# Kernel tuning notes

Measured on AMD Instinct MI355X. Metric: run time of the kernel, lower is better.

Reference implementation:

```python
import jax, jax.numpy as jnp
import numpy as np

D_MODEL = 1024
NUM_HEADS = 16
D_K = D_MODEL // NUM_HEADS
B, S = 4, 2048
NEG = -1e9


def setup_inputs() -> dict:
    key = jax.random.key(0)
    ks = jax.random.split(key, 12)
    def lin(kw, kb):
        bound = 1.0 / np.sqrt(D_MODEL)
        W = jax.random.uniform(kw, (D_MODEL, D_MODEL), jnp.float32, -bound, bound)
        b = jax.random.uniform(kb, (D_MODEL,), jnp.float32, -bound, bound)
        return W, b
    Wq, bq = lin(ks[0], ks[1])
    Wk, bk = lin(ks[2], ks[3])
    Wv, bv = lin(ks[4], ks[5])
    Wo, bo = lin(ks[6], ks[7])
    Q = jax.random.normal(ks[8], (B, S, D_MODEL), jnp.float32)
    K = jax.random.normal(ks[9], (B, S, D_MODEL), jnp.float32)
    V = jax.random.normal(ks[10], (B, S, D_MODEL), jnp.float32)
    # causal mask: 1 = keep, 0 = masked
    mask = jnp.tril(jnp.ones((S, S), jnp.int32))[None, None, :, :]
    mask = jnp.broadcast_to(mask, (B, 1, S, S))
    return {"Q": Q, "K": K, "V": V, "mask": mask,
            "Wq": Wq, "bq": bq, "Wk": Wk, "bk": bk,
            "Wv": Wv, "bv": bv, "Wo": Wo, "bo": bo}


def _split_heads(x):
    b, s, _ = x.shape
    return x.reshape(b, s, NUM_HEADS, D_K).transpose(0, 2, 1, 3)  # [B,H,S,Dk]


def reference(Q, K, V, mask, Wq, bq, Wk, bk, Wv, bv, Wo, bo):
    q = _split_heads(Q @ Wq.T + bq)
    k = _split_heads(K @ Wk.T + bk)
    v = _split_heads(V @ Wv.T + bv)
    scores = jnp.einsum('bhqd,bhkd->bhqk', q, k) / jnp.sqrt(jnp.float32(D_K))
    scores = jnp.where(mask == 0, jnp.float32(NEG), scores)
    probs = jax.nn.softmax(scores, axis=-1)
    attn = jnp.einsum('bhqk,bhkd->bhqd', probs, v)  # [B,H,S,Dk]
    attn = attn.transpose(0, 2, 1, 3).reshape(Q.shape[0], Q.shape[1], D_MODEL)
    return attn @ Wo.T + bo
```

## Files before the change

kernel.cpp:

```cpp
#include <hip/hip_runtime.h>
#include <hip/hip_bf16.h>
#include <cstdint>

typedef float floatx4 __attribute__((ext_vector_type(4)));
typedef __bf16 bf16x8 __attribute__((ext_vector_type(8)));

#define AS_G __attribute__((address_space(1)))
#define AS_L __attribute__((address_space(3)))

__device__ __forceinline__ void async_cp16(const void* g, void* l) {
    __builtin_amdgcn_global_load_lds((const AS_G uint32_t*)g, (AS_L uint32_t*)l, 16, 0, 0);
}

__device__ __forceinline__ floatx4 mfma16x16x32(bf16x8 a, bf16x8 b, floatx4 c) {
    return __builtin_amdgcn_mfma_f32_16x16x32_bf16(a, b, c, 0, 0, 0);
}

__device__ __forceinline__ unsigned short f2bf(float x) {
    return __builtin_bit_cast(unsigned short, (__bf16)x);
}

__global__ __launch_bounds__(256) void cvt4_f32_bf16(const float* __restrict__ a, const float* __restrict__ b,
                                                     const float* __restrict__ c, const float* __restrict__ d,
                                                     unsigned short* __restrict__ out, int n) {
    const float* in = blockIdx.y == 0 ? a : blockIdx.y == 1 ? b : blockIdx.y == 2 ? c : d;
    unsigned short* o = out + (size_t)blockIdx.y * n;
    int i = (blockIdx.x * 256 + threadIdx.x) * 4;
    if (i >= n) return;
    float4 v = *(const float4*)(in + i);
    ushort4 u;
    u.x = f2bf(v.x); u.y = f2bf(v.y); u.z = f2bf(v.z); u.w = f2bf(v.w);
    *(ushort4*)(o + i) = u;
}

__global__ __launch_bounds__(256) void cvt3_f32_bf16(const float* __restrict__ q, const float* __restrict__ k,
                                                     const float* __restrict__ v,
                                                     unsigned short* __restrict__ oq, unsigned short* __restrict__ ok,
                                                     unsigned short* __restrict__ ov, int n) {
    const float* in = blockIdx.y == 0 ? q : blockIdx.y == 1 ? k : v;
    unsigned short* o = blockIdx.y == 0 ? oq : blockIdx.y == 1 ? ok : ov;
    int i = (blockIdx.x * 256 + threadIdx.x) * 4;
    if (i >= n) return;
    float4 f = *(const float4*)(in + i);
    ushort4 u;
    u.x = f2bf(f.x); u.y = f2bf(f.y); u.z = f2bf(f.z); u.w = f2bf(f.w);
    *(ushort4*)(o + i) = u;
}

__device__ __forceinline__ void gemm_core(const unsigned short* __restrict__ A,
                                          const unsigned short* __restrict__ W,
                                          unsigned short* __restrict__ As,
                                          unsigned short* __restrict__ Bs,
                                          int m0, int n0, int wave, int lane,
                                          floatx4 (&acc)[4][4]) {
    const int quad = lane >> 4, l15 = lane & 15;
    const int l7   = l15 & 7;
    const int waveM = (wave >> 1) * 64, waveN = (wave & 1) * 64;
    const int r8  = lane >> 3;
    const int gsw = (lane & 7) ^ r8;

    for (int k0 = 0; k0 < 1024; k0 += 64) {
        for (int c = wave; c < 16; c += 4) {
            const int row = c * 8 + r8;
            async_cp16(A + (size_t)(m0 + row) * 1024 + k0 + gsw * 8, (char*)As + c * 1024);
            async_cp16(W + (size_t)(n0 + row) * 1024 + k0 + gsw * 8, (char*)Bs + c * 1024);
        }
        __syncthreads();

#pragma unroll
        for (int h = 0; h < 2; ++h) {
            const int g = (quad + h * 4) ^ l7;
            bf16x8 af[4], bf[4];
#pragma unroll
            for (int t = 0; t < 4; ++t) {
                af[t] = *(const bf16x8*)&As[(waveM + t * 16 + l15) * 64 + g * 8];
                bf[t] = *(const bf16x8*)&Bs[(waveN + t * 16 + l15) * 64 + g * 8];
            }
#pragma unroll
            for (int mt = 0; mt < 4; ++mt)
#pragma unroll
                for (int nt = 0; nt < 4; ++nt)
                    acc[mt][nt] = mfma16x16x32(af[mt], bf[nt], acc[mt][nt]);
        }
        __syncthreads();
    }
}

__global__ __launch_bounds__(256) void gemm_qkv(const unsigned short* __restrict__ Aq,
                                                const unsigned short* __restrict__ Ak,
                                                const unsigned short* __restrict__ Av,
                                                const unsigned short* __restrict__ wb,
                                                const float* __restrict__ bqp, const float* __restrict__ bkp,
                                                const float* __restrict__ bvp,
                                                float qscl,
                                                unsigned short* __restrict__ qp, unsigned short* __restrict__ kp,
                                                unsigned short* __restrict__ vtp) {
    __shared__ unsigned short As[128 * 64];
    __shared__ unsigned short Bs[128 * 64];
    const int z = blockIdx.z;
    const unsigned short* A = z == 0 ? Aq : z == 1 ? Ak : Av;
    const unsigned short* W = wb + (size_t)z * (1024 * 1024);
    const float* bias = z == 0 ? bqp : z == 1 ? bkp : bvp;
    const float oscale = z == 0 ? qscl : 1.0f;
    unsigned short* out = z == 0 ? qp : z == 1 ? kp : vtp;
    const bool vtrans = (z == 2);

    const int tid  = threadIdx.x;
    const int wave = tid >> 6, lane = tid & 63;
    const int quad = lane >> 4, l15 = lane & 15;
    const int m0 = blockIdx.x * 128, n0 = blockIdx.y * 128;
    const int waveM = (wave >> 1) * 64, waveN = (wave & 1) * 64;

    floatx4 acc[4][4] = {};
    gemm_core(A, W, As, Bs, m0, n0, wave, lane, acc);

#pragma unroll
    for (int mt = 0; mt < 4; ++mt) {
#pragma unroll
        for (int nt = 0; nt < 4; ++nt) {
            const int gcol = n0 + waveN + nt * 16 + l15;
            const float bv = bias[gcol];
#pragma unroll
            for (int r = 0; r < 4; ++r) {
                const int grow = m0 + waveM + mt * 16 + quad * 4 + r;
                const float val = (acc[mt][nt][r] + bv) * oscale;
                const int b = grow >> 11, s = grow & 2047;
                const int h = gcol >> 6, dk = gcol & 63;
                const size_t idx = vtrans ? ((size_t)(b * 16 + h) * 64 + dk) * 2048 + s
                                          : ((size_t)(b * 16 + h) * 2048 + s) * 64 + dk;
                out[idx] = f2bf(val);
            }
        }
    }
}

__global__ __launch_bounds__(256) void gemm_out(const unsigned short* __restrict__ A,
                                                const unsigned short* __restrict__ W,
                                                const float* __restrict__ bias,
                                                float* __restrict__ outv) {
    __shared__ unsigned short As[128 * 64];
    __shared__ unsigned short Bs[128 * 64];
    const int tid  = threadIdx.x;
    const int wave = tid >> 6, lane = tid & 63;
    const int quad = lane >> 4, l15 = lane & 15;
    const int m0 = blockIdx.x * 128, n0 = blockIdx.y * 128;
    const int waveM = (wave >> 1) * 64, waveN = (wave & 1) * 64;

    floatx4 acc[4][4] = {};
    gemm_core(A, W, As, Bs, m0, n0, wave, lane, acc);

#pragma unroll
    for (int mt = 0; mt < 4; ++mt) {
#pragma unroll
        for (int nt = 0; nt < 4; ++nt) {
            const int gcol = n0 + waveN + nt * 16 + l15;
            const float bv = bias[gcol];
#pragma unroll
            for (int r = 0; r < 4; ++r) {
                const int grow = m0 + waveM + mt * 16 + quad * 4 + r;
                outv[(size_t)grow * 1024 + gcol] = acc[mt][nt][r] + bv;
            }
        }
    }
}

#define PS_STRIDE 72

template <bool DIAG>
__device__ __forceinline__ void tile_compute(const bf16x8 kf[4][2], const bf16x8 vf[2][4],
                                             unsigned short* __restrict__ Psw,
                                             bf16x8 qf0, bf16x8 qf1,
                                             int quad, int l15,
                                             int qrow0, int kv0,
                                             float* __restrict__ lsum,
                                             floatx4* __restrict__ O) {
    floatx4 sc[4];
    __builtin_amdgcn_s_setprio(1);
#pragma unroll
    for (int kvt = 0; kvt < 4; ++kvt) {
        floatx4 a = {};
        a = mfma16x16x32(qf0, kf[kvt][0], a);
        a = mfma16x16x32(qf1, kf[kvt][1], a);
        sc[kvt] = a;
    }
    __builtin_amdgcn_s_setprio(0);

#pragma unroll
    for (int kvt = 0; kvt < 4; ++kvt) {
#pragma unroll
        for (int r = 0; r < 4; ++r) {
            float s = sc[kvt][r];
            if (DIAG && (kv0 + kvt * 16 + l15 > qrow0 + r)) s = -1.0e9f;
            const float p = __builtin_amdgcn_exp2f(s);
            lsum[r] += p;
            Psw[(quad * 4 + r) * PS_STRIDE + kvt * 16 + l15] = f2bf(p);
        }
    }

    __builtin_amdgcn_s_setprio(1);
#pragma unroll
    for (int half = 0; half < 2; ++half) {
        bf16x8 pf = *(const bf16x8*)&Psw[l15 * PS_STRIDE + half * 32 + quad * 8];
#pragma unroll
        for (int nt = 0; nt < 4; ++nt)
            O[nt] = mfma16x16x32(pf, vf[half][nt], O[nt]);
    }
    __builtin_amdgcn_s_setprio(0);
}

__global__ __launch_bounds__(256, 3) void flash_causal(const unsigned short* __restrict__ qp,
                                                       const unsigned short* __restrict__ kp,
                                                       const unsigned short* __restrict__ vt,
                                                       unsigned short* __restrict__ attn) {
    __shared__ unsigned short Ks[2][64 * 64];
    __shared__ unsigned short Vs[2][64 * 64];
    __shared__ unsigned short Ps[4 * 16 * PS_STRIDE];

    const int tid  = threadIdx.x;
    const int wave = tid >> 6, lane = tid & 63;
    const int quad = lane >> 4, l15 = lane & 15;
    const int l7   = l15 & 7;
    const int bh = blockIdx.x;
    const int pr = blockIdx.y;
    const int tA = pr, tB = 31 - pr;

    unsigned short* Psw = &Ps[wave * 16 * PS_STRIDE];

    bf16x8 qfA0, qfA1, qfB0, qfB1;
    {
        const unsigned short* qa = qp + ((size_t)bh * 2048 + tA * 64 + wave * 16 + l15) * 64;
        qfA0 = *(const bf16x8*)(qa + quad * 8);
        qfA1 = *(const bf16x8*)(qa + 32 + quad * 8);
        const unsigned short* qb = qp + ((size_t)bh * 2048 + tB * 64 + wave * 16 + l15) * 64;
        qfB0 = *(const bf16x8*)(qb + quad * 8);
        qfB1 = *(const bf16x8*)(qb + 32 + quad * 8);
    }

    float lsumA[4] = {}, lsumB[4] = {};
    floatx4 OA[4] = {}, OB[4] = {};

    const int qrowA = tA * 64 + wave * 16 + quad * 4;
    const int qrowB = tB * 64 + wave * 16 + quad * 4;

    const int r8  = lane >> 3;
    const int gsw = (lane & 7) ^ r8;
    const size_t kb = (size_t)bh * 131072;
    const size_t vb = (size_t)bh * 64 * 2048;

#define STAGE(t, b) do {                                                                  \
        const int kv0_ = (t) * 64;                                                        \
        for (int c = wave; c < 8; c += 4) {                                               \
            const int row_ = c * 8 + r8;                                                  \
            async_cp16(kp + kb + (size_t)(kv0_ + row_) * 64 + gsw * 8,                    \
                       (char*)Ks[b] + c * 1024);                                          \
            async_cp16(vt + vb + (size_t)row_ * 2048 + kv0_ + gsw * 8,                    \
                       (char*)Vs[b] + c * 1024);                                          \
        } } while (0)

    STAGE(0, 0);

    int buf = 0;
    for (int t = 0; t <= tB; ++t) {
        if (t < tB) {
            STAGE(t + 1, buf ^ 1);
            asm volatile("s_waitcnt vmcnt(4)" ::: "memory");
        } else {
            asm volatile("s_waitcnt vmcnt(0)" ::: "memory");
        }
        __builtin_amdgcn_s_barrier();
        __builtin_amdgcn_sched_barrier(0);

        const unsigned short* Kc = Ks[buf];
        const unsigned short* Vc = Vs[buf];

        bf16x8 kf[4][2], vf[2][4];
        const int g1 = quad ^ l7, g2 = (quad + 4) ^ l7;
#pragma unroll
        for (int kvt = 0; kvt < 4; ++kvt) {
            kf[kvt][0] = *(const bf16x8*)&Kc[(kvt * 16 + l15) * 64 + g1 * 8];
            kf[kvt][1] = *(const bf16x8*)&Kc[(kvt * 16 + l15) * 64 + g2 * 8];
        }
#pragma unroll
        for (int half = 0; half < 2; ++half) {
            const int gb = (quad + half * 4) ^ l7;
#pragma unroll
            for (int nt = 0; nt < 4; ++nt)
                vf[half][nt] = *(const bf16x8*)&Vc[(nt * 16 + l15) * 64 + gb * 8];
        }

        const int kv0 = t * 64;
        if (t == tB) tile_compute<true >(kf, vf, Psw, qfB0, qfB1, quad, l15, qrowB, kv0, lsumB, OB);
        else         tile_compute<false>(kf, vf, Psw, qfB0, qfB1, quad, l15, qrowB, kv0, lsumB, OB);
        if (t == tA)      tile_compute<true >(kf, vf, Psw, qfA0, qfA1, quad, l15, qrowA, kv0, lsumA, OA);
        else if (t < tA)  tile_compute<false>(kf, vf, Psw, qfA0, qfA1, quad, l15, qrowA, kv0, lsumA, OA);

        asm volatile("s_waitcnt lgkmcnt(0)" ::: "memory");
        __builtin_amdgcn_sched_barrier(0);
        __builtin_amdgcn_s_barrier();
        buf ^= 1;
    }
#undef STAGE

    const int b = bh >> 4, h = bh & 15;
#pragma unroll
    for (int r = 0; r < 4; ++r) {
        float lA = lsumA[r], lB = lsumB[r];
#pragma unroll
        for (int off = 8; off; off >>= 1) {
            lA += __shfl_xor(lA, off, 16);
            lB += __shfl_xor(lB, off, 16);
        }
        const float invA = 1.0f / lA;
        const float invB = 1.0f / lB;
        const size_t rbA = ((size_t)b * 2048 + qrowA + r) * 1024 + h * 64;
        const size_t rbB = ((size_t)b * 2048 + qrowB + r) * 1024 + h * 64;
#pragma unroll
        for (int nt = 0; nt < 4; ++nt) {
            attn[rbA + nt * 16 + l15] = f2bf(OA[nt][r] * invA);
            attn[rbB + nt * 16 + l15] = f2bf(OB[nt][r] * invB);
        }
    }
}

extern "C" void kernel_launch(void* const* d_in, const int* in_sizes, int n_in,
                              void* d_out, int out_size, void* d_ws, size_t ws_size,
                              hipStream_t stream) {
    const float* Q  = (const float*)d_in[0];
    const float* K  = (const float*)d_in[1];
    const float* V  = (const float*)d_in[2];
    const float* Wq = (const float*)d_in[4];  const float* bq = (const float*)d_in[5];
    const float* Wk = (const float*)d_in[6];  const float* bk = (const float*)d_in[7];
    const float* Wv = (const float*)d_in[8];  const float* bv = (const float*)d_in[9];
    const float* Wo = (const float*)d_in[10]; const float* bo = (const float*)d_in[11];
    float* out = (float*)d_out;

    const int NIN = 8192 * 1024;
    const int NW  = 1024 * 1024;

    unsigned short* ws   = (unsigned short*)d_ws;
    unsigned short* inbV  = ws;
    unsigned short* wb   = inbV + NIN;
    unsigned short* qp   = wb + 4 * NW;
    unsigned short* kp   = qp + NIN;
    unsigned short* vtp  = kp + NIN;
    unsigned short* attnb = vtp + NIN;

    unsigned short* inbQ = (unsigned short*)d_out;
    unsigned short* inbK = inbQ + NIN;

    const float QSCL = 0.125f * 1.44269504088896f;

    dim3 blk(256);
    dim3 gcvtW((NW + 1023) / 1024, 4);
    dim3 gcvtA((NIN + 1023) / 1024, 3);
    dim3 gqkv(64, 8, 3);
    dim3 ggemm(64, 8);
    dim3 gflash(64, 16);

    cvt4_f32_bf16<<<gcvtW, blk, 0, stream>>>(Wq, Wk, Wv, Wo, wb, NW);
    cvt3_f32_bf16<<<gcvtA, blk, 0, stream>>>(Q, K, V, inbQ, inbK, inbV, NIN);

    gemm_qkv<<<gqkv, blk, 0, stream>>>(inbQ, inbK, inbV, wb, bq, bk, bv, QSCL, qp, kp, vtp);

    flash_causal<<<gflash, blk, 0, stream>>>(qp, kp, vtp, attnb);

    gemm_out<<<ggemm, blk, 0, stream>>>(attnb, wb + 3 * NW, bo, out);
}
```

Baseline: 370.6 us.

## Fuse fp32-to-bf16 activation conversion into QKV projection GEMM loads

Drops the separate kernel that converted Q/K/V activations to bf16. Each projection GEMM now reads fp32 activations directly, converts them in registers, and writes them to LDS, with the next k-tile prefetched into registers and custom waitcnt/barrier placement. This removes a full write and re-read of the bf16 activation copies. In exchange the A loads are synchronous register loads rather than async LDS copies, and the fused z-grid launch is split into three separate launches.

After: 364.2 us. Within noise of the previous version (-1.7%).

```diff
diff --git a/kernel.cpp b/kernel.cpp
--- a/kernel.cpp
+++ b/kernel.cpp
@@ -4,6 +4,7 @@
 
 typedef float floatx4 __attribute__((ext_vector_type(4)));
 typedef __bf16 bf16x8 __attribute__((ext_vector_type(8)));
+typedef unsigned short ushort8 __attribute__((ext_vector_type(8)));
 
 #define AS_G __attribute__((address_space(1)))
 #define AS_L __attribute__((address_space(3)))
@@ -33,39 +34,65 @@
     *(ushort4*)(o + i) = u;
 }
 
-__global__ __launch_bounds__(256) void cvt3_f32_bf16(const float* __restrict__ q, const float* __restrict__ k,
-                                                     const float* __restrict__ v,
-                                                     unsigned short* __restrict__ oq, unsigned short* __restrict__ ok,
-                                                     unsigned short* __restrict__ ov, int n) {
-    const float* in = blockIdx.y == 0 ? q : blockIdx.y == 1 ? k : v;
-    unsigned short* o = blockIdx.y == 0 ? oq : blockIdx.y == 1 ? ok : ov;
-    int i = (blockIdx.x * 256 + threadIdx.x) * 4;
-    if (i >= n) return;
-    float4 f = *(const float4*)(in + i);
-    ushort4 u;
-    u.x = f2bf(f.x); u.y = f2bf(f.y); u.z = f2bf(f.z); u.w = f2bf(f.w);
-    *(ushort4*)(o + i) = u;
-}
-
-__device__ __forceinline__ void gemm_core(const unsigned short* __restrict__ A,
-                                          const unsigned short* __restrict__ W,
-                                          unsigned short* __restrict__ As,
-                                          unsigned short* __restrict__ Bs,
-                                          int m0, int n0, int wave, int lane,
-                                          floatx4 (&acc)[4][4]) {
+template <int MODE>
+__global__ __launch_bounds__(256) void gemm_f32a(const float* __restrict__ A,
+                                                 const unsigned short* __restrict__ W,
+                                                 const float* __restrict__ bias,
+                                                 float oscale,
+                                                 unsigned short* __restrict__ outp) {
+    __shared__ unsigned short As[128 * 64];
+    __shared__ unsigned short Bs[128 * 64];
+    const int tid  = threadIdx.x;
+    const int wave = tid >> 6, lane = tid & 63;
     const int quad = lane >> 4, l15 = lane & 15;
     const int l7   = l15 & 7;
+    const int m0 = blockIdx.x * 128, n0 = blockIdx.y * 128;
     const int waveM = (wave >> 1) * 64, waveN = (wave & 1) * 64;
     const int r8  = lane >> 3;
     const int gsw = (lane & 7) ^ r8;
 
+    floatx4 acc[4][4] = {};
+    float4 pre[4][2];
+
+#pragma unroll
+    for (int c4 = 0; c4 < 4; ++c4) {
+        const int row = (wave + c4 * 4) * 8 + r8;
+        const float* src = A + (size_t)(m0 + row) * 1024 + gsw * 8;
+        pre[c4][0] = *(const float4*)src;
+        pre[c4][1] = *(const float4*)(src + 4);
+    }
+
     for (int k0 = 0; k0 < 1024; k0 += 64) {
-        for (int c = wave; c < 16; c += 4) {
+#pragma unroll
+        for (int c4 = 0; c4 < 4; ++c4) {
+            const int c = wave + c4 * 4;
+            ushort8 v;
+            v[0] = f2bf(pre[c4][0].x); v[1] = f2bf(pre[c4][0].y);
+            v[2] = f2bf(pre[c4][0].z); v[3] = f2bf(pre[c4][0].w);
+            v[4] = f2bf(pre[c4][1].x); v[5] = f2bf(pre[c4][1].y);
+            v[6] = f2bf(pre[c4][1].z); v[7] = f2bf(pre[c4][1].w);
+            *(ushort8*)((char*)As + c * 1024 + lane * 16) = v;
+        }
+#pragma unroll
+        for (int c4 = 0; c4 < 4; ++c4) {
+            const int c = wave + c4 * 4;
             const int row = c * 8 + r8;
-            async_cp16(A + (size_t)(m0 + row) * 1024 + k0 + gsw * 8, (char*)As + c * 1024);
             async_cp16(W + (size_t)(n0 + row) * 1024 + k0 + gsw * 8, (char*)Bs + c * 1024);
         }
-        __syncthreads();
+        if (k0 < 960) {
+#pragma unroll
+            for (int c4 = 0; c4 < 4; ++c4) {
+                const int row = (wave + c4 * 4) * 8 + r8;
+                const float* src = A + (size_t)(m0 + row) * 1024 + (k0 + 64) + gsw * 8;
+                pre[c4][0] = *(const float4*)src;
+                pre[c4][1] = *(const float4*)(src + 4);
+            }
+            asm volatile("s_waitcnt vmcnt(8) lgkmcnt(0)" ::: "memory");
+        } else {
+            asm volatile("s_waitcnt vmcnt(0) lgkmcnt(0)" ::: "memory");
+        }
+        __builtin_amdgcn_s_barrier();
+        __builtin_amdgcn_sched_barrier(0);
 
 #pragma unroll
         for (int h = 0; h < 2; ++h) {
@@ -82,37 +109,11 @@
                 for (int nt = 0; nt < 4; ++nt)
                     acc[mt][nt] = mfma16x16x32(af[mt], bf[nt], acc[mt][nt]);
         }
-        __syncthreads();
-    }
-}
-
-__global__ __launch_bounds__(256) void gemm_qkv(const unsigned short* __restrict__ Aq,
-                                                const unsigned short* __restrict__ Ak,
-                                                const unsigned short* __restrict__ Av,
-                                                const unsigned short* __restrict__ wb,
-                                                const float* __restrict__ bqp, const float* __restrict__ bkp,
-                                                const float* __restrict__ bvp,
-                                                float qscl,
-                                                unsigned short* __restrict__ qp, unsigned short* __restrict__ kp,
-                                                unsigned short* __restrict__ vtp) {
-    __shared__ unsigned short As[128 * 64];
-    __shared__ unsigned short Bs[128 * 64];
-    const int z = blockIdx.z;
-    const unsigned short* A = z == 0 ? Aq : z == 1 ? Ak : Av;
-    const unsigned short* W = wb + (size_t)z * (1024 * 1024);
-    const float* bias = z == 0 ? bqp : z == 1 ? bkp : bvp;
-    const float oscale = z == 0 ? qscl : 1.0f;
-    unsigned short* out = z == 0 ? qp : z == 1 ? kp : vtp;
-    const bool vtrans = (z == 2);
-
-    const int tid  = threadIdx.x;
-    const int wave = tid >> 6, lane = tid & 63;
-    const int quad = lane >> 4, l15 = lane & 15;
-    const int m0 = blockIdx.x * 128, n0 = blockIdx.y * 128;
-    const int waveM = (wave >> 1) * 64, waveN = (wave & 1) * 64;
-
-    floatx4 acc[4][4] = {};
-    gemm_core(A, W, As, Bs, m0, n0, wave, lane, acc);
+
+        asm volatile("s_waitcnt lgkmcnt(0)" ::: "memory");
+        __builtin_amdgcn_sched_barrier(0);
+        __builtin_amdgcn_s_barrier();
+    }
 
 #pragma unroll
     for (int mt = 0; mt < 4; ++mt) {
@@ -126,9 +127,9 @@
                 const float val = (acc[mt][nt][r] + bv) * oscale;
                 const int b = grow >> 11, s = grow & 2047;
                 const int h = gcol >> 6, dk = gcol & 63;
-                const size_t idx = vtrans ? ((size_t)(b * 16 + h) * 64 + dk) * 2048 + s
-                                          : ((size_t)(b * 16 + h) * 2048 + s) * 64 + dk;
-                out[idx] = f2bf(val);
+                const size_t idx = (MODE == 1) ? ((size_t)(b * 16 + h) * 64 + dk) * 2048 + s
+                                               : ((size_t)(b * 16 + h) * 2048 + s) * 64 + dk;
+                outp[idx] = f2bf(val);
             }
         }
     }
@@ -143,11 +144,39 @@
     const int tid  = threadIdx.x;
     const int wave = tid >> 6, lane = tid & 63;
     const int quad = lane >> 4, l15 = lane & 15;
+    const int l7   = l15 & 7;
     const int m0 = blockIdx.x * 128, n0 = blockIdx.y * 128;
     const int waveM = (wave >> 1) * 64, waveN = (wave & 1) * 64;
+    const int r8  = lane >> 3;
+    const int gsw = (lane & 7) ^ r8;
 
     floatx4 acc[4][4] = {};
-    gemm_core(A, W, As, Bs, m0, n0, wave, lane, acc);
+
+    for (int k0 = 0; k0 < 1024; k0 += 64) {
+        for (int c = wave; c < 16; c += 4) {
+            const int row = c * 8 + r8;
+            async_cp16(A + (size_t)(m0 + row) * 1024 + k0 + gsw * 8, (char*)As + c * 1024);
+            async_cp16(W + (size_t)(n0 + row) * 1024 + k0 + gsw * 8, (char*)Bs + c * 1024);
+        }
+        __syncthreads();
+
+#pragma unroll
+        for (int h = 0; h < 2; ++h) {
+            const int g = (quad + h * 4) ^ l7;
+            bf16x8 af[4], bf[4];
+#pragma unroll
+            for (int t = 0; t < 4; ++t) {
+                af[t] = *(const bf16x8*)&As[(waveM + t * 16 + l15) * 64 + g * 8];
+                bf[t] = *(const bf16x8*)&Bs[(waveN + t * 16 + l15) * 64 + g * 8];
+            }
+#pragma unroll
+            for (int mt = 0; mt < 4; ++mt)
+#pragma unroll
+                for (int nt = 0; nt < 4; ++nt)
+                    acc[mt][nt] = mfma16x16x32(af[mt], bf[nt], acc[mt][nt]);
+        }
+        __syncthreads();
+    }
 
 #pragma unroll
     for (int mt = 0; mt < 4; ++mt) {
@@ -338,29 +367,24 @@
     const int NW  = 1024 * 1024;
 
     unsigned short* ws   = (unsigned short*)d_ws;
-    unsigned short* inbV  = ws;
-    unsigned short* wb   = inbV + NIN;
+    unsigned short* wb   = ws;
     unsigned short* qp   = wb + 4 * NW;
     unsigned short* kp   = qp + NIN;
     unsigned short* vtp  = kp + NIN;
     unsigned short* attnb = vtp + NIN;
 
-    unsigned short* inbQ = (unsigned short*)d_out;
-    unsigned short* inbK = inbQ + NIN;
-
     const float QSCL = 0.125f * 1.44269504088896f;
 
     dim3 blk(256);
     dim3 gcvtW((NW + 1023) / 1024, 4);
-    dim3 gcvtA((NIN + 1023) / 1024, 3);
-    dim3 gqkv(64, 8, 3);
     dim3 ggemm(64, 8);
     dim3 gflash(64, 16);
 
     cvt4_f32_bf16<<<gcvtW, blk, 0, stream>>>(Wq, Wk, Wv, Wo, wb, NW);
-    cvt3_f32_bf16<<<gcvtA, blk, 0, stream>>>(Q, K, V, inbQ, inbK, inbV, NIN);
-
-    gemm_qkv<<<gqkv, blk, 0, stream>>>(inbQ, inbK, inbV, wb, bq, bk, bv, QSCL, qp, kp, vtp);
+
+    gemm_f32a<0><<<ggemm, blk, 0, stream>>>(Q, wb + 0 * NW, bq, QSCL, qp);
+    gemm_f32a<0><<<ggemm, blk, 0, stream>>>(K, wb + 1 * NW, bk, 1.0f, kp);
+    gemm_f32a<1><<<ggemm, blk, 0, stream>>>(V, wb + 2 * NW, bv, 1.0f, vtp);
 
     flash_causal<<<gflash, blk, 0, stream>>>(qp, kp, vtp, attnb);
 
```
